# Optimization experiments

Hardware: AMD Instinct MI355X
Metric: run time of the kernel (lower is better)

## Reference

```python
import jax, jax.numpy as jnp
import numpy as np

B = 8192
MAX_ATOMS = 768
EPS = 1e-7


def setup_inputs() -> dict:
    key = jax.random.key(0)
    k1, k2, k3 = jax.random.split(key, 3)
    inp = jax.random.normal(k1, (B, 3 * MAX_ATOMS), dtype=jnp.float32)
    tgt = jax.random.normal(k2, (B, 3 * MAX_ATOMS), dtype=jnp.float32)
    # variable atom counts; keep >= MAX_ATOMS//2 so centering/division is well-posed
    num_atoms = jax.random.randint(k3, (B,), MAX_ATOMS // 2, MAX_ATOMS + 1, dtype=jnp.int64)
    return {"input": inp, "target": tgt, "num_atoms": num_atoms}


def _kabsch_rmsd(inp, tgt, num_atoms):
    b = inp.shape[0]
    m = inp.shape[1] // 3
    X = inp.reshape(b, m, 3)
    Y = tgt.reshape(b, m, 3)
    mask = (jnp.arange(m)[None, :] < num_atoms[:, None])[..., None]  # [B, M, 1]
    n = num_atoms.astype(inp.dtype)[:, None]  # [B, 1]
    # center over the valid atoms of each sample
    Xc = (X - (jnp.where(mask, X, 0).sum(axis=1) / n)[:, None, :])
    Yc = (Y - (jnp.where(mask, Y, 0).sum(axis=1) / n)[:, None, :])
    Xc = jnp.where(mask, Xc, 0)
    Yc = jnp.where(mask, Yc, 0)
    # 3x3 correlation matrix per sample (Kabsch)
    R = jnp.einsum('bai,baj->bij', Xc, Yc)  # [B, 3, 3]
    s = jnp.linalg.svd(R, compute_uv=False)  # [B, 3], descending
    d = jnp.sign(jnp.linalg.det(R))  # proper-rotation correction
    trace = s[:, 0] + s[:, 1] + d * s[:, 2]
    e = jnp.sum(Xc * Xc, axis=(1, 2)) + jnp.sum(Yc * Yc, axis=(1, 2)) - 2.0 * trace
    n1 = num_atoms.astype(inp.dtype)
    return jnp.sqrt(jnp.maximum(e, 0.0) / n1 + EPS)


def reference(input, target, num_atoms):
    return _kabsch_rmsd(input, target, num_atoms)
```

## Files before the change

kernel.cpp:

```cpp
#include <hip/hip_runtime.h>
#include <math.h>

#ifndef M_PI
#define M_PI 3.14159265358979323846
#endif

#define MA 768

__device__ __forceinline__ float dpp_red_add(float v) {
    v += __int_as_float(__builtin_amdgcn_update_dpp(0, __float_as_int(v), 0x111, 0xf, 0xf, true));
    v += __int_as_float(__builtin_amdgcn_update_dpp(0, __float_as_int(v), 0x112, 0xf, 0xf, true));
    v += __int_as_float(__builtin_amdgcn_update_dpp(0, __float_as_int(v), 0x114, 0xf, 0xe, true));
    v += __int_as_float(__builtin_amdgcn_update_dpp(0, __float_as_int(v), 0x118, 0xf, 0xc, true));
    v += __int_as_float(__builtin_amdgcn_update_dpp(0, __float_as_int(v), 0x142, 0xa, 0xf, true));
    v += __int_as_float(__builtin_amdgcn_update_dpp(0, __float_as_int(v), 0x143, 0xc, 0xf, true));
    return v;
}

__global__ __launch_bounds__(256, 4) void kabsch_kernel(
    const float* __restrict__ inp, const float* __restrict__ tgt,
    const int* __restrict__ natoms, float* __restrict__ out)
{
    const int wave = threadIdx.x >> 6;
    const int lane = threadIdx.x & 63;
    const int b = blockIdx.x * 4 + wave;
    const int n = natoms[b];
    const float* __restrict__ X = inp + (size_t)b * (3 * MA);
    const float* __restrict__ Y = tgt + (size_t)b * (3 * MA);

    const int a0 = 12 * lane;

    const float4 f4z = make_float4(0.f, 0.f, 0.f, 0.f);
    float4 vx[9], vy[9];
#pragma unroll
    for (int k = 0; k < 9; ++k) { vx[k] = f4z; vy[k] = f4z; }

    if (a0 < n) {
        const float4* px = (const float4*)(X + 3 * a0);
        const float4* py = (const float4*)(Y + 3 * a0);
#pragma unroll
        for (int k = 0; k < 9; ++k) vx[k] = px[k];
#pragma unroll
        for (int k = 0; k < 9; ++k) vy[k] = py[k];
    }
    __builtin_amdgcn_sched_barrier(0);

    float ax[36], ay[36];
#pragma unroll
    for (int k = 0; k < 9; ++k) {
        *(float4*)&ax[4 * k] = vx[k];
        *(float4*)&ay[4 * k] = vy[k];
    }

    float sx0 = 0.f, sx1 = 0.f, sx2 = 0.f;
    float sy0 = 0.f, sy1 = 0.f, sy2 = 0.f;
    float c00 = 0.f, c01 = 0.f, c02 = 0.f;
    float c10 = 0.f, c11 = 0.f, c12 = 0.f;
    float c20 = 0.f, c21 = 0.f, c22 = 0.f;
    float nx2 = 0.f, ny2 = 0.f;

#pragma unroll
    for (int j = 0; j < 12; ++j) {
        const bool v = (a0 + j) < n;
        const float x0 = v ? ax[3 * j + 0] : 0.f;
        const float x1 = v ? ax[3 * j + 1] : 0.f;
        const float x2 = v ? ax[3 * j + 2] : 0.f;
        const float y0 = v ? ay[3 * j + 0] : 0.f;
        const float y1 = v ? ay[3 * j + 1] : 0.f;
        const float y2 = v ? ay[3 * j + 2] : 0.f;
        sx0 += x0; sx1 += x1; sx2 += x2;
        sy0 += y0; sy1 += y1; sy2 += y2;
        c00 = fmaf(x0, y0, c00); c01 = fmaf(x0, y1, c01); c02 = fmaf(x0, y2, c02);
        c10 = fmaf(x1, y0, c10); c11 = fmaf(x1, y1, c11); c12 = fmaf(x1, y2, c12);
        c20 = fmaf(x2, y0, c20); c21 = fmaf(x2, y1, c21); c22 = fmaf(x2, y2, c22);
        nx2 = fmaf(x0, x0, nx2); nx2 = fmaf(x1, x1, nx2); nx2 = fmaf(x2, x2, nx2);
        ny2 = fmaf(y0, y0, ny2); ny2 = fmaf(y1, y1, ny2); ny2 = fmaf(y2, y2, ny2);
    }

    sx0 = dpp_red_add(sx0); sx1 = dpp_red_add(sx1); sx2 = dpp_red_add(sx2);
    sy0 = dpp_red_add(sy0); sy1 = dpp_red_add(sy1); sy2 = dpp_red_add(sy2);
    c00 = dpp_red_add(c00); c01 = dpp_red_add(c01); c02 = dpp_red_add(c02);
    c10 = dpp_red_add(c10); c11 = dpp_red_add(c11); c12 = dpp_red_add(c12);
    c20 = dpp_red_add(c20); c21 = dpp_red_add(c21); c22 = dpp_red_add(c22);
    nx2 = dpp_red_add(nx2); ny2 = dpp_red_add(ny2);

    if (lane == 63) {
        const double inv_n = 1.0 / (double)n;

        double R00 = (double)c00 - (double)sx0 * (double)sy0 * inv_n;
        double R01 = (double)c01 - (double)sx0 * (double)sy1 * inv_n;
        double R02 = (double)c02 - (double)sx0 * (double)sy2 * inv_n;
        double R10 = (double)c10 - (double)sx1 * (double)sy0 * inv_n;
        double R11 = (double)c11 - (double)sx1 * (double)sy1 * inv_n;
        double R12 = (double)c12 - (double)sx1 * (double)sy2 * inv_n;
        double R20 = (double)c20 - (double)sx2 * (double)sy0 * inv_n;
        double R21 = (double)c21 - (double)sx2 * (double)sy1 * inv_n;
        double R22 = (double)c22 - (double)sx2 * (double)sy2 * inv_n;
        double ex = (double)nx2 -
            ((double)sx0 * sx0 + (double)sx1 * sx1 + (double)sx2 * sx2) * inv_n;
        double ey = (double)ny2 -
            ((double)sy0 * sy0 + (double)sy1 * sy1 + (double)sy2 * sy2) * inv_n;

        double A00 = R00 * R00 + R10 * R10 + R20 * R20;
        double A11 = R01 * R01 + R11 * R11 + R21 * R21;
        double A22 = R02 * R02 + R12 * R12 + R22 * R22;
        double A01 = R00 * R01 + R10 * R11 + R20 * R21;
        double A02 = R00 * R02 + R10 * R12 + R20 * R22;
        double A12 = R01 * R02 + R11 * R12 + R21 * R22;

        double detR = R00 * (R11 * R22 - R12 * R21)
                    - R01 * (R10 * R22 - R12 * R20)
                    + R02 * (R10 * R21 - R11 * R20);

        double q = (A00 + A11 + A22) / 3.0;
        double p1 = A01 * A01 + A02 * A02 + A12 * A12;
        double b00 = A00 - q, b11 = A11 - q, b22 = A22 - q;
        double p2 = b00 * b00 + b11 * b11 + b22 * b22 + 2.0 * p1;
        double e0, e1, e2;
        if (p2 <= 0.0) {
            e0 = e1 = e2 = q;
        } else {
            double p = sqrt(p2 / 6.0);
            double ip = 1.0 / p;
            double B00 = b00 * ip, B11 = b11 * ip, B22 = b22 * ip;
            double B01 = A01 * ip, B02 = A02 * ip, B12 = A12 * ip;
            double detB = B00 * (B11 * B22 - B12 * B12)
                        - B01 * (B01 * B22 - B12 * B02)
                        + B02 * (B01 * B12 - B11 * B02);
            double r = 0.5 * detB;
            r = fmin(1.0, fmax(-1.0, r));
            float phi = acosf((float)r) * (1.0f / 3.0f);
            float cA = __cosf(phi);
            float cC = __cosf(phi + (float)(2.0 * M_PI / 3.0));
            e0 = q + 2.0 * p * (double)cA;
            e2 = q + 2.0 * p * (double)cC;
            e1 = 3.0 * q - e0 - e2;
        }
        double s0 = sqrt(fmax(e0, 0.0));
        double s1 = sqrt(fmax(e1, 0.0));
        double s2 = sqrt(fmax(e2, 0.0));
        double d = (detR > 0.0) ? 1.0 : ((detR < 0.0) ? -1.0 : 0.0);
        double tr = s0 + s1 + d * s2;
        double e = ex + ey - 2.0 * tr;
        out[b] = (float)sqrt(fmax(e, 0.0) * inv_n + 1e-7);
    }
}

extern "C" void kernel_launch(void* const* d_in, const int* in_sizes, int n_in,
                              void* d_out, int out_size, void* d_ws, size_t ws_size,
                              hipStream_t stream) {
    const float* inp = (const float*)d_in[0];
    const float* tgt = (const float*)d_in[1];
    const int* natoms = (const int*)d_in[2];
    float* out = (float*)d_out;
    (void)d_ws; (void)ws_size; (void)n_in; (void)in_sizes;
    kabsch_kernel<<<dim3(out_size / 4), dim3(256), 0, stream>>>(inp, tgt, natoms, out);
}
```

Baseline: 25.13 us.

## Use coalesced interleaved float loads with neighbor-window Y and skip inactive chunks

Each lane used to load 12 contiguous atoms, 36 floats per row, so a wave's loads were strided. Now each wave reads the row in 256-float chunks, each lane taking one float4 of X. It also reads two overlapping float4 windows of Y so it can form the cross products for its atom components, and reassigns the partial sums by lane%3 before the DPP reductions. Chunks past the valid atom count are skipped with per-wave branches, and the later loads are interleaved with consumption of earlier chunks. In exchange it loads Y twice (redundant bandwidth, largely cache hits) and adds extra selects and registers.

```diff
diff --git a/kernel.cpp b/kernel.cpp
--- a/kernel.cpp
+++ b/kernel.cpp
@@ -6,6 +6,7 @@
 #endif
 
 #define MA 768
+#define ROWF (3 * MA)
 
 __device__ __forceinline__ float dpp_red_add(float v) {
     v += __int_as_float(__builtin_amdgcn_update_dpp(0, __float_as_int(v), 0x111, 0xf, 0xf, true));
@@ -17,6 +18,63 @@
     return v;
 }
 
+struct Acc {
+    float sxp[3], syp[3], cp[3][3], nx2, ny2;
+};
+
+template<int K, bool MASK, bool FIRST, bool LAST>
+__device__ __forceinline__ void consume(const float4& xr, const float4& ya,
+                                        const float4& yb, int pl, int nf,
+                                        bool r1, bool r2, bool lane0,
+                                        bool lane63, Acc& A)
+{
+    float yc[8] = {ya.x, ya.y, ya.z, ya.w, yb.x, yb.y, yb.z, yb.w};
+    if (FIRST) {
+        yc[2] = lane0 ? ya.x : ya.z;
+        yc[3] = lane0 ? ya.y : ya.w;
+    }
+    if (LAST) {
+        yc[4] = lane63 ? yb.z : yb.x;
+        yc[5] = lane63 ? yb.w : yb.y;
+    }
+    const float xe[4] = {xr.x, xr.y, xr.z, xr.w};
+#pragma unroll
+    for (int e = 0; e < 4; ++e) {
+        float x = xe[e];
+        float yal = yc[e + 2];
+        if (MASK) {
+            const bool v = (256 * K + pl + e) < nf;
+            x = v ? x : 0.f;
+            yal = v ? yal : 0.f;
+        }
+        const int m = (K + e) % 3;
+        A.sxp[m] += x;
+        A.syp[m] += yal;
+        A.nx2 = fmaf(x, x, A.nx2);
+        A.ny2 = fmaf(yal, yal, A.ny2);
+#pragma unroll
+        for (int j = 0; j < 3; ++j) {
+            const int c0 = e + 2 - m + j;
+            const int c1 = e + 2 - ((m + 1) % 3) + j;
+            const int c2 = e + 2 - ((m + 2) % 3) + j;
+            const float yj = r1 ? yc[c1] : (r2 ? yc[c2] : yc[c0]);
+            A.cp[m][j] = fmaf(x, yj, A.cp[m][j]);
+        }
+    }
+}
+
+#define LOADK(K, xv, av, bv)                                              \
+    {                                                                     \
+        const int xo = 256 * (K) + pl;                                    \
+        int ao = xo - 2;                                                  \
+        if ((K) == 0 && ao < 0) ao = 0;                                   \
+        int bo = xo + 2;                                                  \
+        if ((K) == 8 && bo > ROWF - 4) bo = ROWF - 4;                     \
+        xv = *(const float4*)(X + xo);                                    \
+        av = *(const float4*)(Y + ao);                                    \
+        bv = *(const float4*)(Y + bo);                                    \
+    }
+
 __global__ __launch_bounds__(256, 4) void kabsch_kernel(
     const float* __restrict__ inp, const float* __restrict__ tgt,
     const int* __restrict__ natoms, float* __restrict__ out)
@@ -25,66 +83,68 @@
     const int lane = threadIdx.x & 63;
     const int b = blockIdx.x * 4 + wave;
     const int n = natoms[b];
-    const float* __restrict__ X = inp + (size_t)b * (3 * MA);
-    const float* __restrict__ Y = tgt + (size_t)b * (3 * MA);
-
-    const int a0 = 12 * lane;
-
-    const float4 f4z = make_float4(0.f, 0.f, 0.f, 0.f);
-    float4 vx[9], vy[9];
-#pragma unroll
-    for (int k = 0; k < 9; ++k) { vx[k] = f4z; vy[k] = f4z; }
-
-    if (a0 < n) {
-        const float4* px = (const float4*)(X + 3 * a0);
-        const float4* py = (const float4*)(Y + 3 * a0);
-#pragma unroll
-        for (int k = 0; k < 9; ++k) vx[k] = px[k];
-#pragma unroll
-        for (int k = 0; k < 9; ++k) vy[k] = py[k];
-    }
+    const int nf = 3 * n;
+    const float* __restrict__ X = inp + (size_t)b * ROWF;
+    const float* __restrict__ Y = tgt + (size_t)b * ROWF;
+
+    const int pl = 4 * lane;
+    const int r = lane % 3;
+    const bool r1 = (r == 1), r2 = (r == 2);
+    const bool lane0 = (lane == 0), lane63 = (lane == 63);
+
+    Acc A;
+#pragma unroll
+    for (int m = 0; m < 3; ++m) {
+        A.sxp[m] = 0.f; A.syp[m] = 0.f;
+#pragma unroll
+        for (int j = 0; j < 3; ++j) A.cp[m][j] = 0.f;
+    }
+    A.nx2 = 0.f; A.ny2 = 0.f;
+
+    float4 x0, a0, b0, x1, a1, b1, x2, a2, b2, x3, a3, b3, x4, a4, b4;
+    LOADK(0, x0, a0, b0);
+    LOADK(1, x1, a1, b1);
+    LOADK(2, x2, a2, b2);
+    LOADK(3, x3, a3, b3);
+    LOADK(4, x4, a4, b4);
     __builtin_amdgcn_sched_barrier(0);
 
-    float ax[36], ay[36];
-#pragma unroll
-    for (int k = 0; k < 9; ++k) {
-        *(float4*)&ax[4 * k] = vx[k];
-        *(float4*)&ay[4 * k] = vy[k];
-    }
-
-    float sx0 = 0.f, sx1 = 0.f, sx2 = 0.f;
-    float sy0 = 0.f, sy1 = 0.f, sy2 = 0.f;
-    float c00 = 0.f, c01 = 0.f, c02 = 0.f;
-    float c10 = 0.f, c11 = 0.f, c12 = 0.f;
-    float c20 = 0.f, c21 = 0.f, c22 = 0.f;
-    float nx2 = 0.f, ny2 = 0.f;
-
-#pragma unroll
-    for (int j = 0; j < 12; ++j) {
-        const bool v = (a0 + j) < n;
-        const float x0 = v ? ax[3 * j + 0] : 0.f;
-        const float x1 = v ? ax[3 * j + 1] : 0.f;
-        const float x2 = v ? ax[3 * j + 2] : 0.f;
-        const float y0 = v ? ay[3 * j + 0] : 0.f;
-        const float y1 = v ? ay[3 * j + 1] : 0.f;
-        const float y2 = v ? ay[3 * j + 2] : 0.f;
-        sx0 += x0; sx1 += x1; sx2 += x2;
-        sy0 += y0; sy1 += y1; sy2 += y2;
-        c00 = fmaf(x0, y0, c00); c01 = fmaf(x0, y1, c01); c02 = fmaf(x0, y2, c02);
-        c10 = fmaf(x1, y0, c10); c11 = fmaf(x1, y1, c11); c12 = fmaf(x1, y2, c12);
-        c20 = fmaf(x2, y0, c20); c21 = fmaf(x2, y1, c21); c22 = fmaf(x2, y2, c22);
-        nx2 = fmaf(x0, x0, nx2); nx2 = fmaf(x1, x1, nx2); nx2 = fmaf(x2, x2, nx2);
-        ny2 = fmaf(y0, y0, ny2); ny2 = fmaf(y1, y1, ny2); ny2 = fmaf(y2, y2, ny2);
-    }
-
-    sx0 = dpp_red_add(sx0); sx1 = dpp_red_add(sx1); sx2 = dpp_red_add(sx2);
-    sy0 = dpp_red_add(sy0); sy1 = dpp_red_add(sy1); sy2 = dpp_red_add(sy2);
-    c00 = dpp_red_add(c00); c01 = dpp_red_add(c01); c02 = dpp_red_add(c02);
-    c10 = dpp_red_add(c10); c11 = dpp_red_add(c11); c12 = dpp_red_add(c12);
-    c20 = dpp_red_add(c20); c21 = dpp_red_add(c21); c22 = dpp_red_add(c22);
-    nx2 = dpp_red_add(nx2); ny2 = dpp_red_add(ny2);
-
-    if (lane == 63) {
+    float4 x5, a5, b5, x6, a6, b6, x7, a7, b7, x8, a8, b8;
+    const bool k5 = nf > 1280, k6 = nf > 1536, k7 = nf > 1792, k8 = nf > 2048;
+
+    if (k5) LOADK(5, x5, a5, b5);
+    consume<0, false, true, false>(x0, a0, b0, pl, nf, r1, r2, lane0, lane63, A);
+    if (k6) LOADK(6, x6, a6, b6);
+    consume<1, false, false, false>(x1, a1, b1, pl, nf, r1, r2, lane0, lane63, A);
+    if (k7) LOADK(7, x7, a7, b7);
+    consume<2, false, false, false>(x2, a2, b2, pl, nf, r1, r2, lane0, lane63, A);
+    if (k8) LOADK(8, x8, a8, b8);
+    consume<3, false, false, false>(x3, a3, b3, pl, nf, r1, r2, lane0, lane63, A);
+    consume<4, true, false, false>(x4, a4, b4, pl, nf, r1, r2, lane0, lane63, A);
+    if (k5) consume<5, true, false, false>(x5, a5, b5, pl, nf, r1, r2, lane0, lane63, A);
+    if (k6) consume<6, true, false, false>(x6, a6, b6, pl, nf, r1, r2, lane0, lane63, A);
+    if (k7) consume<7, true, false, false>(x7, a7, b7, pl, nf, r1, r2, lane0, lane63, A);
+    if (k8) consume<8, true, false, true>(x8, a8, b8, pl, nf, r1, r2, lane0, lane63, A);
+
+    float sx[3], sy[3], c[3][3];
+#pragma unroll
+    for (int i = 0; i < 3; ++i) {
+        const int q0 = i, q1 = (i + 2) % 3, q2 = (i + 1) % 3;
+        sx[i] = r1 ? A.sxp[q1] : (r2 ? A.sxp[q2] : A.sxp[q0]);
+        sy[i] = r1 ? A.syp[q1] : (r2 ? A.syp[q2] : A.syp[q0]);
+#pragma unroll
+        for (int j = 0; j < 3; ++j)
+            c[i][j] = r1 ? A.cp[q1][j] : (r2 ? A.cp[q2][j] : A.cp[q0][j]);
+    }
+
+    const float sx0 = dpp_red_add(sx[0]), sx1 = dpp_red_add(sx[1]), sx2 = dpp_red_add(sx[2]);
+    const float sy0 = dpp_red_add(sy[0]), sy1 = dpp_red_add(sy[1]), sy2 = dpp_red_add(sy[2]);
+    const float c00 = dpp_red_add(c[0][0]), c01 = dpp_red_add(c[0][1]), c02 = dpp_red_add(c[0][2]);
+    const float c10 = dpp_red_add(c[1][0]), c11 = dpp_red_add(c[1][1]), c12 = dpp_red_add(c[1][2]);
+    const float c20 = dpp_red_add(c[2][0]), c21 = dpp_red_add(c[2][1]), c22 = dpp_red_add(c[2][2]);
+    const float nx2 = dpp_red_add(A.nx2), ny2 = dpp_red_add(A.ny2);
+
+    if (lane63) {
         const double inv_n = 1.0 / (double)n;
 
         double R00 = (double)c00 - (double)sx0 * (double)sy0 * inv_n;
@@ -127,9 +187,9 @@
             double detB = B00 * (B11 * B22 - B12 * B12)
                         - B01 * (B01 * B22 - B12 * B02)
                         + B02 * (B01 * B12 - B11 * B02);
-            double r = 0.5 * detB;
-            r = fmin(1.0, fmax(-1.0, r));
-            float phi = acosf((float)r) * (1.0f / 3.0f);
+            double rr = 0.5 * detB;
+            rr = fmin(1.0, fmax(-1.0, rr));
+            float phi = acosf((float)rr) * (1.0f / 3.0f);
             float cA = __cosf(phi);
             float cC = __cosf(phi + (float)(2.0 * M_PI / 3.0));
             e0 = q + 2.0 * p * (double)cA;
```

Result: slower. 28.72 us (+14.3%).
